# Kernel optimization log

Measured on AMD Instinct MI355X. Metric: run time of the kernel, lower is better.

## Reference

```python
import jax, jax.numpy as jnp
import numpy as np

N, IN_DIM, D, H, OUT = 4096, 512, 256, 256, 128


def setup_inputs() -> dict:
    key = jax.random.key(0)
    ks = jax.random.split(key, 12)
    s = 0.05
    x = jax.random.normal(ks[0], (N, IN_DIM), dtype=jnp.float32)
    # sparse-ish dense adjacency mask (avg degree ~80), int since only adj>0 is used
    adj = (jax.random.uniform(ks[1], (N, N)) < 0.02).astype(jnp.int32)
    return {
        "x": x,
        "adj": adj,
        "lin1_w": jax.random.normal(ks[2], (D, IN_DIM), dtype=jnp.float32) * s,
        "lin1_b": jax.random.normal(ks[3], (D,), dtype=jnp.float32) * s,
        "gat_W": jax.random.normal(ks[4], (D, D), dtype=jnp.float32) * s,
        "a_self": jax.random.normal(ks[5], (D,), dtype=jnp.float32) * s,
        "a_neigh": jax.random.normal(ks[6], (D,), dtype=jnp.float32) * s,
        "W_ih": jax.random.normal(ks[7], (4 * H, D), dtype=jnp.float32) * s,
        "W_hh": jax.random.normal(ks[8], (4 * H, H), dtype=jnp.float32) * s,
        "lin2_w": jax.random.normal(ks[9], (OUT, D), dtype=jnp.float32) * s,
        "lin2_b": jax.random.normal(ks[10], (OUT,), dtype=jnp.float32) * s,
    }


def reference(x, adj, lin1_w, lin1_b, gat_W, a_self, a_neigh, W_ih, W_hh, lin2_w, lin2_b):
    M = jnp.float32(0.2)        # scalar M passed by EWNELayer
    LRELU_SLOPE = 0.2           # alpha given to GraphAttentionLayer
    NEG_INF = jnp.float32(-9e15)

    # lin1
    x1 = x @ lin1_w.T + lin1_b                       # [N, D]

    # --- GraphAttentionLayer (DAEGC-style, dense adjacency mask) ---
    h = x1 @ gat_W                                   # [N, D]
    e = (h @ a_self)[:, None] + (h @ a_neigh)[None, :]  # [N, N]
    e = jax.nn.leaky_relu(e * M, LRELU_SLOPE)
    scores = jnp.where(adj > 0, e, NEG_INF)
    attn = jax.nn.softmax(scores, axis=1)            # [N, N]
    h_prime = attn @ h                               # [N, D]
    g = jnp.tanh(jax.nn.elu(h_prime))                # ELU (concat=True) then tanh

    # --- single-timestep LSTM, no bias, h0 = c0 = 0 ---
    h0 = jnp.zeros((N, H), dtype=g.dtype)
    c0 = jnp.zeros((N, H), dtype=g.dtype)
    gates = g @ W_ih.T + h0 @ W_hh.T                 # [N, 4H], torch order i,f,g,o
    i_g, f_g, g_g, o_g = jnp.split(gates, 4, axis=1)
    i_g = jax.nn.sigmoid(i_g)
    f_g = jax.nn.sigmoid(f_g)
    g_g = jnp.tanh(g_g)
    o_g = jax.nn.sigmoid(o_g)
    c1 = f_g * c0 + i_g * g_g
    h1 = o_g * jnp.tanh(c1)                          # [N, H]

    # lin2 -> normalize -> dot-product decode
    out = h1 @ lin2_w.T + lin2_b                     # [N, OUT]
    norm = jnp.maximum(jnp.linalg.norm(out, axis=1, keepdims=True), 1e-12)
    z = out / norm
    A_pred = jax.nn.sigmoid(z @ z.T)                 # [N, N]
    return A_pred, z, out
```

## Files before the change

### kernel.cpp

```cpp
#include <hip/hip_runtime.h>

#define NN_ 4096
#define IN_DIM_ 512
#define D_ 256
#define OUT_ 128
#define MAXC 320

typedef unsigned short u16;
typedef unsigned int u32;
typedef __attribute__((ext_vector_type(8))) short short8;
typedef __attribute__((ext_vector_type(4))) float f32x4;
typedef __attribute__((ext_vector_type(4))) int i32x4;

union U16x8 { uint4 u4; short8 s8; };

__device__ __forceinline__ u16 f2bf(float f){
  u32 u = __builtin_bit_cast(u32, f);
  u = (u + 0x7FFFu + ((u >> 16) & 1u)) >> 16;
  return (u16)u;
}
__device__ __forceinline__ float bf2f(u16 u){ return __builtin_bit_cast(float, ((u32)u) << 16); }
__device__ __forceinline__ float sigm(float v){ return __fdividef(1.f, 1.f + __expf(-v)); }

__device__ __forceinline__ void mfma_mainloop(const u16* __restrict__ A,
    const u16* __restrict__ B, int K, int ldA, int ldB, int row0, int col0,
    uint4* As, uint4* Bs, f32x4 acc[4][4], int tid) {
  const int wave = tid >> 6, lane = tid & 63;
  const int wm = wave >> 1, wn = wave & 1;
  const int r16 = lane & 15, kg = lane >> 4;
  for (int k0 = 0; k0 < K; k0 += 64) {
    #pragma unroll
    for (int i = 0; i < 4; i++) {
      int id = tid + (i << 8);
      int r = id >> 3, cc = id & 7;
      As[(r << 3) + (cc ^ (r & 7))] = *(const uint4*)(A + (size_t)(row0 + r) * ldA + k0 + cc * 8);
      Bs[(r << 3) + (cc ^ (r & 7))] = *(const uint4*)(B + (size_t)(col0 + r) * ldB + k0 + cc * 8);
    }
    __syncthreads();
    #pragma unroll
    for (int ks = 0; ks < 2; ks++) {
      int kb = (ks << 2) + kg;
      U16x8 a[4], b[4];
      #pragma unroll
      for (int m2 = 0; m2 < 4; m2++) {
        int r = (wm << 6) + (m2 << 4) + r16;
        a[m2].u4 = As[(r << 3) + (kb ^ (r & 7))];
      }
      #pragma unroll
      for (int n2 = 0; n2 < 4; n2++) {
        int r = (wn << 6) + (n2 << 4) + r16;
        b[n2].u4 = Bs[(r << 3) + (kb ^ (r & 7))];
      }
      #pragma unroll
      for (int m2 = 0; m2 < 4; m2++)
        #pragma unroll
        for (int n2 = 0; n2 < 4; n2++)
          acc[m2][n2] = __builtin_amdgcn_mfma_f32_16x16x32_bf16(
              a[m2].s8, b[n2].s8, acc[m2][n2], 0, 0, 0);
    }
    __syncthreads();
  }
}

__global__ __launch_bounds__(256) void prep_kernel(
    const float* __restrict__ lin1_w, const float* __restrict__ gat_W,
    const float* __restrict__ lin1_b,
    u16* __restrict__ WcT_bf, float* __restrict__ bcomb) {
  __shared__ __align__(16) float As[32][36];
  __shared__ __align__(16) float Bs[32][36];
  const int b = blockIdx.x, tid = threadIdx.x;
  if (b < 128) {
    const int m0 = (b & 15) << 5;
    const int n0 = (b >> 4) << 5;
    const int tx = tid & 15, ty = tid >> 4;
    float acc[2][2] = {};
    for (int k0 = 0; k0 < 256; k0 += 32) {
      int kk = tid >> 3, c4 = (tid & 7) << 2;
      *(float4*)&As[kk][c4] = *(const float4*)(lin1_w + (size_t)(k0 + kk) * 512 + m0 + c4);
      *(float4*)&Bs[kk][c4] = *(const float4*)(gat_W + (size_t)(k0 + kk) * 256 + n0 + c4);
      __syncthreads();
      #pragma unroll
      for (int k2 = 0; k2 < 32; k2++) {
        float a0 = As[k2][(ty << 1)], a1 = As[k2][(ty << 1) + 1];
        float b0 = Bs[k2][(tx << 1)], b1 = Bs[k2][(tx << 1) + 1];
        acc[0][0] = __builtin_fmaf(a0, b0, acc[0][0]);
        acc[0][1] = __builtin_fmaf(a0, b1, acc[0][1]);
        acc[1][0] = __builtin_fmaf(a1, b0, acc[1][0]);
        acc[1][1] = __builtin_fmaf(a1, b1, acc[1][1]);
      }
      __syncthreads();
    }
    #pragma unroll
    for (int r = 0; r < 2; r++)
      #pragma unroll
      for (int c = 0; c < 2; c++)
        WcT_bf[(size_t)(n0 + (tx << 1) + c) * 512 + m0 + (ty << 1) + r] = f2bf(acc[r][c]);
  } else {
    float a = 0.f;
    #pragma unroll 8
    for (int d = 0; d < 256; d++)
      a = __builtin_fmaf(lin1_b[d], gat_W[(size_t)d * 256 + tid], a);
    bcomb[tid] = a;
  }
}

__global__ __launch_bounds__(256) void hgemm_st_kernel(const float* __restrict__ x,
    const u16* __restrict__ WcT, const float* __restrict__ bias,
    const float* __restrict__ a_self, const float* __restrict__ a_nei,
    const float* __restrict__ W_ih, const float* __restrict__ lin2_w,
    const int* __restrict__ adj,
    u16* __restrict__ h_bf, float* __restrict__ s, float* __restrict__ t,
    u16* __restrict__ Wihp_bf, u16* __restrict__ l2w_bf,
    u16* __restrict__ nidxg, int* __restrict__ cnt) {
  __shared__ uint4 As[16 * 8];
  __shared__ uint4 Bs[256 * 8];
  __shared__ float sred[4][16];
  __shared__ float tred[4][16];
  __shared__ int wtot4[4];
  const int tid = threadIdx.x;
  int b = blockIdx.x;
  if (b >= 480) {
    const int row = b - 480;
    const int lane = tid & 63, wave = tid >> 6;
    const i32x4* arow = (const i32x4*)(adj + (size_t)row * NN_);
    i32x4 a4[4];
    #pragma unroll
    for (int i = 0; i < 4; i++) a4[i] = __builtin_nontemporal_load(&arow[(i << 8) + tid]);
    int vals[16];
    #pragma unroll
    for (int i = 0; i < 4; i++)
      #pragma unroll
      for (int q = 0; q < 4; q++) vals[(i << 2) + q] = a4[i][q];
    int c = 0;
    #pragma unroll
    for (int q = 0; q < 16; q++) c += (vals[q] > 0);
    int pref = c;
    #pragma unroll
    for (int off = 1; off < 64; off <<= 1) {
      int u = __shfl_up(pref, off);
      if (lane >= off) pref += u;
    }
    if (lane == 63) wtot4[wave] = pref;
    __syncthreads();
    int woff = 0;
    #pragma unroll
    for (int w = 0; w < 4; w++) woff += (w < wave) ? wtot4[w] : 0;
    int n = wtot4[0] + wtot4[1] + wtot4[2] + wtot4[3];
    int p = woff + pref - c;
    #pragma unroll
    for (int i = 0; i < 4; i++)
      #pragma unroll
      for (int q = 0; q < 4; q++) {
        if (vals[(i << 2) + q] > 0) {
          int j = (i << 10) + (tid << 2) + q;
          if (p < MAXC) nidxg[(size_t)row * MAXC + p] = (u16)j;
          p++;
        }
      }
    if (tid == 0) cnt[row] = n;
    return;
  }
  if (b >= 256) {
    b -= 256;
    if (b < 192) {
      int r = (b << 2) + (tid >> 6);
      int grp = r / 48, rem = r - grp * 48;
      int gidx = rem >> 4, hcl = rem & 15;
      int gate = (gidx == 0) ? 0 : ((gidx == 1) ? 2 : 3);
      int orig = gate * 256 + grp * 16 + hcl;
      int k = (tid & 63) << 2;
      float4 v = *(const float4*)(W_ih + (size_t)orig * 256 + k);
      ushort4 o = {f2bf(v.x), f2bf(v.y), f2bf(v.z), f2bf(v.w)};
      *(ushort4*)(Wihp_bf + (size_t)r * 256 + k) = o;
    } else {
      int off = (b - 192) * 1024 + tid * 4;
      float4 v = *(const float4*)(lin2_w + off);
      ushort4 o = {f2bf(v.x), f2bf(v.y), f2bf(v.z), f2bf(v.w)};
      *(ushort4*)(l2w_bf + off) = o;
    }
    return;
  }
  const int row0 = b << 4;
  const int wave = tid >> 6, lane = tid & 63;
  const int r16 = lane & 15, kg = lane >> 4;
  f32x4 acc[4];
  #pragma unroll
  for (int n2 = 0; n2 < 4; n2++) acc[n2] = (f32x4){0.f,0.f,0.f,0.f};
  for (int k0 = 0; k0 < IN_DIM_; k0 += 64) {
    if (tid < 128) {
      int r = tid >> 3, cc = tid & 7;
      const float* src = x + (size_t)(row0 + r) * IN_DIM_ + k0 + cc * 8;
      float4 lo = *(const float4*)src;
      float4 hi = *(const float4*)(src + 4);
      u16 e[8] = {f2bf(lo.x), f2bf(lo.y), f2bf(lo.z), f2bf(lo.w),
                  f2bf(hi.x), f2bf(hi.y), f2bf(hi.z), f2bf(hi.w)};
      As[(r << 3) + (cc ^ (r & 7))] = *(uint4*)e;
    }
    #pragma unroll
    for (int i = 0; i < 8; i++) {
      int id = tid + (i << 8);
      int r = id >> 3, cc = id & 7;
      Bs[(r << 3) + (cc ^ (r & 7))] = *(const uint4*)(WcT + (size_t)r * IN_DIM_ + k0 + cc * 8);
    }
    __syncthreads();
    #pragma unroll
    for (int ks = 0; ks < 2; ks++) {
      int kb = (ks << 2) + kg;
      U16x8 a, bb[4];
      a.u4 = As[(r16 << 3) + (kb ^ (r16 & 7))];
      #pragma unroll
      for (int n2 = 0; n2 < 4; n2++) {
        int r = (wave << 6) + (n2 << 4) + r16;
        bb[n2].u4 = Bs[(r << 3) + (kb ^ (r & 7))];
      }
      #pragma unroll
      for (int n2 = 0; n2 < 4; n2++)
        acc[n2] = __builtin_amdgcn_mfma_f32_16x16x32_bf16(a.s8, bb[n2].s8, acc[n2], 0, 0, 0);
    }
    __syncthreads();
  }
  float ps[4] = {0.f,0.f,0.f,0.f}, pt[4] = {0.f,0.f,0.f,0.f};
  #pragma unroll
  for (int n2 = 0; n2 < 4; n2++) {
    int col = (wave << 6) + (n2 << 4) + r16;
    float as = a_self[col], an = a_nei[col], bs = bias[col];
    #pragma unroll
    for (int q = 0; q < 4; q++) {
      float v = acc[n2][q] + bs;
      h_bf[(size_t)(row0 + (kg << 2) + q) * D_ + col] = f2bf(v);
      ps[q] = __builtin_fmaf(v, as, ps[q]);
      pt[q] = __builtin_fmaf(v, an, pt[q]);
    }
  }
  #pragma unroll
  for (int q = 0; q < 4; q++) {
    #pragma unroll
    for (int off = 8; off; off >>= 1) {
      ps[q] += __shfl_xor(ps[q], off);
      pt[q] += __shfl_xor(pt[q], off);
    }
  }
  if (r16 == 0) {
    #pragma unroll
    for (int q = 0; q < 4; q++) {
      sred[wave][(kg << 2) + q] = ps[q];
      tred[wave][(kg << 2) + q] = pt[q];
    }
  }
  __syncthreads();
  if (tid < 16)
    s[row0 + tid] = sred[0][tid] + sred[1][tid] + sred[2][tid] + sred[3][tid];
  else if (tid < 32)
    t[row0 + tid - 16] = tred[0][tid-16] + tred[1][tid-16] + tred[2][tid-16] + tred[3][tid-16];
}

__global__ __launch_bounds__(256) void attn4_kernel(const u16* __restrict__ nidxg,
    const int* __restrict__ cnt, const u16* __restrict__ h_bf,
    const float* __restrict__ s, const float* __restrict__ t,
    u16* __restrict__ g_bf) {
  __shared__ int nidx[MAXC];
  __shared__ float ne[MAXC];
  __shared__ float red[4][256];
  __shared__ float reds[4];
  const int tid = threadIdx.x;
  const int row = blockIdx.x;
  const int lane = tid & 63, wave = tid >> 6;
  int n = cnt[row];
  if (n > MAXC) n = MAXC;
  const float si = s[row];
  float ls = 0.f;
  for (int k = tid; k < n; k += 256) {
    int j = nidxg[(size_t)row * MAXC + k];
    float e = 0.2f * (si + t[j]);
    e = e > 0.f ? e : 0.2f * e;
    float wgt = __expf(e);
    nidx[k] = j; ne[k] = wgt; ls += wgt;
  }
  #pragma unroll
  for (int off = 32; off; off >>= 1) ls += __shfl_xor(ls, off);
  if (lane == 0) reds[wave] = ls;
  __syncthreads();
  float S = reds[0] + reds[1] + reds[2] + reds[3];
  const int hl = lane & 31, ksel = lane >> 5;
  float acc[8] = {0.f, 0.f, 0.f, 0.f, 0.f, 0.f, 0.f, 0.f};
  #pragma unroll 4
  for (int k = (wave << 1) + ksel; k < n; k += 8) {
    float wgt = ne[k];
    int j = nidx[k];
    U16x8 hv; hv.u4 = *(const uint4*)(h_bf + ((size_t)j << 8) + (hl << 3));
    #pragma unroll
    for (int q = 0; q < 8; q++)
      acc[q] = __builtin_fmaf(wgt, bf2f((u16)hv.s8[q]), acc[q]);
  }
  #pragma unroll
  for (int q = 0; q < 8; q++) acc[q] += __shfl_down(acc[q], 32);
  if (lane < 32) {
    #pragma unroll
    for (int q = 0; q < 8; q++) red[wave][(hl << 3) + q] = acc[q];
  }
  __syncthreads();
  float hp;
  if (n > 0) {
    hp = (red[0][tid] + red[1][tid] + red[2][tid] + red[3][tid]) / S;
  } else {
    float a2 = 0.f;
    for (int j = 0; j < NN_; j++) a2 += bf2f(h_bf[((size_t)j << 8) + tid]);
    hp = a2 / NN_;
  }
  float el = hp > 0.f ? hp : __expf(hp) - 1.f;
  g_bf[((size_t)row << 8) + tid] = f2bf(tanhf(el));
}

__global__ __launch_bounds__(256) void gates_lstm_kernel(const u16* __restrict__ A,
    const u16* __restrict__ B, u16* __restrict__ h1b) {
  __shared__ uint4 As[128 * 8];
  __shared__ uint4 Bs[96 * 8];
  const int tid = threadIdx.x;
  const int row0 = blockIdx.y << 7;
  const int col0 = blockIdx.x * 96;
  const int wave = tid >> 6, lane = tid & 63;
  const int wm = wave >> 1, wn = wave & 1;
  const int r16 = lane & 15, kg = lane >> 4;
  f32x4 acc[4][3];
  #pragma unroll
  for (int m2 = 0; m2 < 4; m2++)
    #pragma unroll
    for (int n2 = 0; n2 < 3; n2++) acc[m2][n2] = (f32x4){0.f,0.f,0.f,0.f};
  for (int k0 = 0; k0 < D_; k0 += 64) {
    #pragma unroll
    for (int i = 0; i < 4; i++) {
      int id = tid + (i << 8);
      int r = id >> 3, cc = id & 7;
      As[(r << 3) + (cc ^ (r & 7))] = *(const uint4*)(A + (size_t)(row0 + r) * D_ + k0 + cc * 8);
    }
    #pragma unroll
    for (int i = 0; i < 3; i++) {
      int id = tid + (i << 8);
      int r = id >> 3, cc = id & 7;
      Bs[(r << 3) + (cc ^ (r & 7))] = *(const uint4*)(B + (size_t)(col0 + r) * D_ + k0 + cc * 8);
    }
    __syncthreads();
    #pragma unroll
    for (int ks = 0; ks < 2; ks++) {
      int kb = (ks << 2) + kg;
      U16x8 a[4], bb[3];
      #pragma unroll
      for (int m2 = 0; m2 < 4; m2++) {
        int r = (wm << 6) + (m2 << 4) + r16;
        a[m2].u4 = As[(r << 3) + (kb ^ (r & 7))];
      }
      #pragma unroll
      for (int n2 = 0; n2 < 3; n2++) {
        int r = wn * 48 + (n2 << 4) + r16;
        bb[n2].u4 = Bs[(r << 3) + (kb ^ (r & 7))];
      }
      #pragma unroll
      for (int m2 = 0; m2 < 4; m2++)
        #pragma unroll
        for (int n2 = 0; n2 < 3; n2++)
          acc[m2][n2] = __builtin_amdgcn_mfma_f32_16x16x32_bf16(
              a[m2].s8, bb[n2].s8, acc[m2][n2], 0, 0, 0);
    }
    __syncthreads();
  }
  const int hc = ((blockIdx.x << 1) + wn) * 16 + r16;
  #pragma unroll
  for (int m2 = 0; m2 < 4; m2++)
    #pragma unroll
    for (int q = 0; q < 4; q++) {
      size_t grow = row0 + (wm << 6) + (m2 << 4) + (kg << 2) + q;
      float ig = acc[m2][0][q], gg = acc[m2][1][q], og = acc[m2][2][q];
      float c1 = sigm(ig) * tanhf(gg);
      h1b[grow * D_ + hc] = f2bf(sigm(og) * tanhf(c1));
    }
}

__global__ __launch_bounds__(256) void lin2f_kernel(const u16* __restrict__ A,
    const u16* __restrict__ B, const float* __restrict__ bias,
    float* __restrict__ out, float* __restrict__ z, u16* __restrict__ zb) {
  __shared__ uint4 As[16 * 8];
  __shared__ uint4 Bs[128 * 8];
  __shared__ float ssred[4][16];
  const int tid = threadIdx.x;
  const int wave = tid >> 6, lane = tid & 63;
  const int r16 = lane & 15, kg = lane >> 4;
  const int row0 = blockIdx.x << 4;
  f32x4 acc[2];
  acc[0] = (f32x4){0.f,0.f,0.f,0.f}; acc[1] = (f32x4){0.f,0.f,0.f,0.f};
  for (int k0 = 0; k0 < D_; k0 += 64) {
    if (tid < 128) {
      int r = tid >> 3, cc = tid & 7;
      As[(r << 3) + (cc ^ (r & 7))] = *(const uint4*)(A + (size_t)(row0 + r) * D_ + k0 + cc * 8);
    }
    #pragma unroll
    for (int i = 0; i < 4; i++) {
      int id = tid + (i << 8);
      int r = id >> 3, cc = id & 7;
      Bs[(r << 3) + (cc ^ (r & 7))] = *(const uint4*)(B + (size_t)r * D_ + k0 + cc * 8);
    }
    __syncthreads();
    #pragma unroll
    for (int ks = 0; ks < 2; ks++) {
      int kb = (ks << 2) + kg;
      U16x8 a, bb[2];
      a.u4 = As[(r16 << 3) + (kb ^ (r16 & 7))];
      #pragma unroll
      for (int n2 = 0; n2 < 2; n2++) {
        int r = (wave << 5) + (n2 << 4) + r16;
        bb[n2].u4 = Bs[(r << 3) + (kb ^ (r & 7))];
      }
      #pragma unroll
      for (int n2 = 0; n2 < 2; n2++)
        acc[n2] = __builtin_amdgcn_mfma_f32_16x16x32_bf16(a.s8, bb[n2].s8, acc[n2], 0, 0, 0);
    }
    __syncthreads();
  }
  float v[2][4], ss[4];
  #pragma unroll
  for (int q = 0; q < 4; q++) ss[q] = 0.f;
  #pragma unroll
  for (int n2 = 0; n2 < 2; n2++) {
    int col = (wave << 5) + (n2 << 4) + r16;
    float bs = bias[col];
    #pragma unroll
    for (int q = 0; q < 4; q++) {
      float vv = acc[n2][q] + bs;
      v[n2][q] = vv;
      ss[q] = __builtin_fmaf(vv, vv, ss[q]);
    }
  }
  #pragma unroll
  for (int q = 0; q < 4; q++)
    #pragma unroll
    for (int off = 8; off; off >>= 1) ss[q] += __shfl_xor(ss[q], off);
  if (r16 == 0) {
    #pragma unroll
    for (int q = 0; q < 4; q++) ssred[wave][(kg << 2) + q] = ss[q];
  }
  __syncthreads();
  #pragma unroll
  for (int q = 0; q < 4; q++) {
    int rrow = (kg << 2) + q;
    float tot = ssred[0][rrow] + ssred[1][rrow] + ssred[2][rrow] + ssred[3][rrow];
    float inv = __fdividef(1.f, fmaxf(sqrtf(tot), 1e-12f));
    size_t grow = row0 + rrow;
    #pragma unroll
    for (int n2 = 0; n2 < 2; n2++) {
      int col = (wave << 5) + (n2 << 4) + r16;
      float vv = v[n2][q], zz = vv * inv;
      out[grow * OUT_ + col] = vv;
      z[grow * OUT_ + col] = zz;
      zb[grow * OUT_ + col] = f2bf(zz);
    }
  }
}

__global__ __launch_bounds__(256) void decode_kernel(const u16* __restrict__ zb,
    float* __restrict__ C) {
  __shared__ uint4 As[128 * 8];
  __shared__ uint4 Bs[128 * 8];
  const int tid = threadIdx.x;
  const int row0 = blockIdx.y << 7, col0 = blockIdx.x << 7;
  f32x4 acc[4][4];
  #pragma unroll
  for (int m2 = 0; m2 < 4; m2++)
    #pragma unroll
    for (int n2 = 0; n2 < 4; n2++) acc[m2][n2] = (f32x4){0.f,0.f,0.f,0.f};
  mfma_mainloop(zb, zb, OUT_, OUT_, OUT_, row0, col0, As, Bs, acc, tid);
  const int wave = tid >> 6, lane = tid & 63;
  const int r16 = lane & 15, kg = lane >> 4;
  const int orow = row0 + ((wave >> 1) << 6), ocol = col0 + ((wave & 1) << 6);
  #pragma unroll
  for (int m2 = 0; m2 < 4; m2++)
    #pragma unroll
    for (int n2 = 0; n2 < 4; n2++)
      #pragma unroll
      for (int q = 0; q < 4; q++) {
        size_t gr = orow + (m2 << 4) + (kg << 2) + q;
        int gc = ocol + (n2 << 4) + r16;
        C[gr * NN_ + gc] = sigm(acc[m2][n2][q]);
      }
}

extern "C" void kernel_launch(void* const* d_in, const int* in_sizes, int n_in,
                              void* d_out, int out_size, void* d_ws, size_t ws_size,
                              hipStream_t stream) {
  const float* x      = (const float*)d_in[0];
  const int*   adj    = (const int*)  d_in[1];
  const float* lin1_w = (const float*)d_in[2];
  const float* lin1_b = (const float*)d_in[3];
  const float* gat_W  = (const float*)d_in[4];
  const float* a_self = (const float*)d_in[5];
  const float* a_nei  = (const float*)d_in[6];
  const float* W_ih   = (const float*)d_in[7];
  const float* lin2_w = (const float*)d_in[9];
  const float* lin2_b = (const float*)d_in[10];

  float* A_pred = (float*)d_out;
  float* z_out  = A_pred + (size_t)NN_ * NN_;
  float* out_o  = z_out + (size_t)NN_ * OUT_;

  char* w = (char*)d_ws;
  u16* h_bf    = (u16*)w;
  u16* g_bf    = (u16*)(w + (2u << 20));
  u16* h1_bf   = (u16*)(w + (4u << 20));
  u16* zb      = (u16*)(w + (6u << 20));
  u16* Wihp_bf = (u16*)(w + (7u << 20));
  u16* WcT_bf  = (u16*)(w + (7u << 20) + (384u << 10));
  u16* l2w_bf  = (u16*)(w + (7u << 20) + (640u << 10));
  float* bcomb = (float*)(w + (7u << 20) + (704u << 10));
  float* s     = (float*)(w + (7u << 20) + (768u << 10));
  float* t     = (float*)(w + (7u << 20) + (832u << 10));
  u16* nidxg   = (u16*)(w + (8u << 20));
  int* cnt     = (int*)(w + (11u << 20));

  prep_kernel<<<dim3(129), dim3(256), 0, stream>>>(
      lin1_w, gat_W, lin1_b, WcT_bf, bcomb);
  hgemm_st_kernel<<<dim3(4576), dim3(256), 0, stream>>>(
      x, WcT_bf, bcomb, a_self, a_nei, W_ih, lin2_w, adj,
      h_bf, s, t, Wihp_bf, l2w_bf, nidxg, cnt);
  attn4_kernel<<<dim3(4096), dim3(256), 0, stream>>>(nidxg, cnt, h_bf, s, t, g_bf);
  gates_lstm_kernel<<<dim3(8, 32), dim3(256), 0, stream>>>(g_bf, Wihp_bf, h1_bf);
  lin2f_kernel<<<dim3(256), dim3(256), 0, stream>>>(h1_bf, l2w_bf, lin2_b, out_o, z_out, zb);
  decode_kernel<<<dim3(32, 32), dim3(256), 0, stream>>>(zb, A_pred);
}
```

Before: 80.09 us.

## Fuse LSTM gates GEMM with lin2/normalize kernel keeping h1 in LDS

Merges the gates+LSTM GEMM and the lin2+L2-normalize GEMM into one 512-thread kernel that processes 64 rows per block. The h1 activations stay in shared memory instead of a global round trip, and one kernel launch is removed. It also reorders the hgemm_st grid so the adjacency-compaction blocks come first. The catch is only 64 blocks on a large GPU, so parallelism is low and there is more LDS per block.

```diff
diff --git a/kernel.cpp b/kernel.cpp
--- a/kernel.cpp
+++ b/kernel.cpp
@@ -119,8 +119,8 @@
   __shared__ int wtot4[4];
   const int tid = threadIdx.x;
   int b = blockIdx.x;
-  if (b >= 480) {
-    const int row = b - 480;
+  if (b < 4096) {
+    const int row = b;
     const int lane = tid & 63, wave = tid >> 6;
     const i32x4* arow = (const i32x4*)(adj + (size_t)row * NN_);
     i32x4 a4[4];
@@ -160,6 +160,7 @@
     if (tid == 0) cnt[row] = n;
     return;
   }
+  b -= 4096;
   if (b >= 256) {
     b -= 256;
     if (b < 192) {
@@ -311,148 +312,170 @@
   g_bf[((size_t)row << 8) + tid] = f2bf(tanhf(el));
 }
 
-__global__ __launch_bounds__(256) void gates_lstm_kernel(const u16* __restrict__ A,
-    const u16* __restrict__ B, u16* __restrict__ h1b) {
-  __shared__ uint4 As[128 * 8];
-  __shared__ uint4 Bs[96 * 8];
-  const int tid = threadIdx.x;
-  const int row0 = blockIdx.y << 7;
-  const int col0 = blockIdx.x * 96;
-  const int wave = tid >> 6, lane = tid & 63;
-  const int wm = wave >> 1, wn = wave & 1;
-  const int r16 = lane & 15, kg = lane >> 4;
-  f32x4 acc[4][3];
-  #pragma unroll
-  for (int m2 = 0; m2 < 4; m2++)
-    #pragma unroll
-    for (int n2 = 0; n2 < 3; n2++) acc[m2][n2] = (f32x4){0.f,0.f,0.f,0.f};
-  for (int k0 = 0; k0 < D_; k0 += 64) {
-    #pragma unroll
-    for (int i = 0; i < 4; i++) {
-      int id = tid + (i << 8);
-      int r = id >> 3, cc = id & 7;
-      As[(r << 3) + (cc ^ (r & 7))] = *(const uint4*)(A + (size_t)(row0 + r) * D_ + k0 + cc * 8);
-    }
-    #pragma unroll
-    for (int i = 0; i < 3; i++) {
-      int id = tid + (i << 8);
-      int r = id >> 3, cc = id & 7;
-      Bs[(r << 3) + (cc ^ (r & 7))] = *(const uint4*)(B + (size_t)(col0 + r) * D_ + k0 + cc * 8);
-    }
-    __syncthreads();
-    #pragma unroll
-    for (int ks = 0; ks < 2; ks++) {
-      int kb = (ks << 2) + kg;
-      U16x8 a[4], bb[3];
-      #pragma unroll
-      for (int m2 = 0; m2 < 4; m2++) {
-        int r = (wm << 6) + (m2 << 4) + r16;
-        a[m2].u4 = As[(r << 3) + (kb ^ (r & 7))];
-      }
-      #pragma unroll
-      for (int n2 = 0; n2 < 3; n2++) {
-        int r = wn * 48 + (n2 << 4) + r16;
-        bb[n2].u4 = Bs[(r << 3) + (kb ^ (r & 7))];
-      }
-      #pragma unroll
-      for (int m2 = 0; m2 < 4; m2++)
-        #pragma unroll
-        for (int n2 = 0; n2 < 3; n2++)
-          acc[m2][n2] = __builtin_amdgcn_mfma_f32_16x16x32_bf16(
-              a[m2].s8, bb[n2].s8, acc[m2][n2], 0, 0, 0);
-    }
-    __syncthreads();
-  }
-  const int hc = ((blockIdx.x << 1) + wn) * 16 + r16;
-  #pragma unroll
-  for (int m2 = 0; m2 < 4; m2++)
-    #pragma unroll
-    for (int q = 0; q < 4; q++) {
-      size_t grow = row0 + (wm << 6) + (m2 << 4) + (kg << 2) + q;
-      float ig = acc[m2][0][q], gg = acc[m2][1][q], og = acc[m2][2][q];
-      float c1 = sigm(ig) * tanhf(gg);
-      h1b[grow * D_ + hc] = f2bf(sigm(og) * tanhf(c1));
-    }
-}
-
-__global__ __launch_bounds__(256) void lin2f_kernel(const u16* __restrict__ A,
-    const u16* __restrict__ B, const float* __restrict__ bias,
-    float* __restrict__ out, float* __restrict__ z, u16* __restrict__ zb) {
-  __shared__ uint4 As[16 * 8];
-  __shared__ uint4 Bs[128 * 8];
-  __shared__ float ssred[4][16];
+__global__ __launch_bounds__(512) void glf_kernel(const u16* __restrict__ g_bf,
+    const u16* __restrict__ Wihp, const u16* __restrict__ l2w,
+    const float* __restrict__ bias, float* __restrict__ out,
+    float* __restrict__ z, u16* __restrict__ zb) {
+  __shared__ uint4 As[64 * 32];
+  __shared__ uint4 Bs[384 * 8];
+  __shared__ u16 h1s[64 * 256];
+  __shared__ float ssred[8][32];
   const int tid = threadIdx.x;
   const int wave = tid >> 6, lane = tid & 63;
+  const int wm = wave >> 2, wn = wave & 3;
   const int r16 = lane & 15, kg = lane >> 4;
-  const int row0 = blockIdx.x << 4;
-  f32x4 acc[2];
-  acc[0] = (f32x4){0.f,0.f,0.f,0.f}; acc[1] = (f32x4){0.f,0.f,0.f,0.f};
+  const int r0 = blockIdx.x << 6;
+  #pragma unroll
+  for (int i = 0; i < 4; i++) {
+    int e = tid + (i << 9);
+    int r = e >> 5, kb = e & 31;
+    As[(r << 5) + (kb ^ (r & 7))] = *(const uint4*)(g_bf + (size_t)(r0 + r) * D_ + kb * 8);
+  }
+  for (int p = 0; p < 2; p++) {
+    f32x4 acc[2][6];
+    #pragma unroll
+    for (int m2 = 0; m2 < 2; m2++)
+      #pragma unroll
+      for (int n2 = 0; n2 < 6; n2++) acc[m2][n2] = (f32x4){0.f,0.f,0.f,0.f};
+    for (int k0 = 0; k0 < D_; k0 += 64) {
+      #pragma unroll
+      for (int i = 0; i < 6; i++) {
+        int e = tid + (i << 9);
+        int r = e >> 3, c8 = e & 7;
+        Bs[(r << 3) + (c8 ^ (r & 7))] =
+            *(const uint4*)(Wihp + (size_t)(p * 384 + r) * D_ + k0 + c8 * 8);
+      }
+      __syncthreads();
+      #pragma unroll
+      for (int ks = 0; ks < 2; ks++) {
+        int kbi = (k0 >> 3) + (ks << 2) + kg;
+        int kb8 = (ks << 2) + kg;
+        U16x8 a[2], bb[6];
+        #pragma unroll
+        for (int m2 = 0; m2 < 2; m2++) {
+          int r = (wm << 5) + (m2 << 4) + r16;
+          a[m2].u4 = As[(r << 5) + (kbi ^ (r & 7))];
+        }
+        #pragma unroll
+        for (int n2 = 0; n2 < 6; n2++) {
+          int rl = wn * 96 + (n2 << 4) + r16;
+          bb[n2].u4 = Bs[(rl << 3) + (kb8 ^ (rl & 7))];
+        }
+        #pragma unroll
+        for (int m2 = 0; m2 < 2; m2++)
+          #pragma unroll
+          for (int n2 = 0; n2 < 6; n2++)
+            acc[m2][n2] = __builtin_amdgcn_mfma_f32_16x16x32_bf16(
+                a[m2].s8, bb[n2].s8, acc[m2][n2], 0, 0, 0);
+      }
+      __syncthreads();
+    }
+    #pragma unroll
+    for (int m2 = 0; m2 < 2; m2++)
+      #pragma unroll
+      for (int g2 = 0; g2 < 2; g2++) {
+        int hc = (((p << 3) + (wn << 1) + g2) << 4) + r16;
+        int u = hc >> 3, sub = hc & 7;
+        #pragma unroll
+        for (int q = 0; q < 4; q++) {
+          int r = (wm << 5) + (m2 << 4) + (kg << 2) + q;
+          float i_ = acc[m2][g2 * 3 + 0][q];
+          float g_ = acc[m2][g2 * 3 + 1][q];
+          float o_ = acc[m2][g2 * 3 + 2][q];
+          float c1 = sigm(i_) * tanhf(g_);
+          h1s[((r << 5) + (u ^ (r & 7))) * 8 + sub] = f2bf(sigm(o_) * tanhf(c1));
+        }
+      }
+  }
+  __syncthreads();
+  const uint4* h1v = (const uint4*)h1s;
+  f32x4 acc2[2][2];
+  #pragma unroll
+  for (int m2 = 0; m2 < 2; m2++)
+    #pragma unroll
+    for (int n2 = 0; n2 < 2; n2++) acc2[m2][n2] = (f32x4){0.f,0.f,0.f,0.f};
   for (int k0 = 0; k0 < D_; k0 += 64) {
-    if (tid < 128) {
-      int r = tid >> 3, cc = tid & 7;
-      As[(r << 3) + (cc ^ (r & 7))] = *(const uint4*)(A + (size_t)(row0 + r) * D_ + k0 + cc * 8);
-    }
-    #pragma unroll
-    for (int i = 0; i < 4; i++) {
-      int id = tid + (i << 8);
-      int r = id >> 3, cc = id & 7;
-      Bs[(r << 3) + (cc ^ (r & 7))] = *(const uint4*)(B + (size_t)r * D_ + k0 + cc * 8);
+    #pragma unroll
+    for (int i = 0; i < 2; i++) {
+      int e = tid + (i << 9);
+      int r = e >> 3, c8 = e & 7;
+      Bs[(r << 3) + (c8 ^ (r & 7))] = *(const uint4*)(l2w + (size_t)r * D_ + k0 + c8 * 8);
     }
     __syncthreads();
     #pragma unroll
     for (int ks = 0; ks < 2; ks++) {
-      int kb = (ks << 2) + kg;
-      U16x8 a, bb[2];
-      a.u4 = As[(r16 << 3) + (kb ^ (r16 & 7))];
+      int kbi = (k0 >> 3) + (ks << 2) + kg;
+      int kb8 = (ks << 2) + kg;
+      U16x8 a[2], bb[2];
+      #pragma unroll
+      for (int m2 = 0; m2 < 2; m2++) {
+        int r = (wm << 5) + (m2 << 4) + r16;
+        a[m2].u4 = h1v[(r << 5) + (kbi ^ (r & 7))];
+      }
       #pragma unroll
       for (int n2 = 0; n2 < 2; n2++) {
-        int r = (wave << 5) + (n2 << 4) + r16;
-        bb[n2].u4 = Bs[(r << 3) + (kb ^ (r & 7))];
-      }
-      #pragma unroll
-      for (int n2 = 0; n2 < 2; n2++)
-        acc[n2] = __builtin_amdgcn_mfma_f32_16x16x32_bf16(a.s8, bb[n2].s8, acc[n2], 0, 0, 0);
-    }
-    __syncthreads();
-  }
-  float v[2][4], ss[4];
-  #pragma unroll
-  for (int q = 0; q < 4; q++) ss[q] = 0.f;
-  #pragma unroll
-  for (int n2 = 0; n2 < 2; n2++) {
-    int col = (wave << 5) + (n2 << 4) + r16;
-    float bs = bias[col];
+        int rl = (wn << 5) + (n2 << 4) + r16;
+        bb[n2].u4 = Bs[(rl << 3) + (kb8 ^ (rl & 7))];
+      }
+      #pragma unroll
+      for (int m2 = 0; m2 < 2; m2++)
+        #pragma unroll
+        for (int n2 = 0; n2 < 2; n2++)
+          acc2[m2][n2] = __builtin_amdgcn_mfma_f32_16x16x32_bf16(
+              a[m2].s8, bb[n2].s8, acc2[m2][n2], 0, 0, 0);
+    }
+    __syncthreads();
+  }
+  float v[2][2][4], ss[2][4];
+  #pragma unroll
+  for (int m2 = 0; m2 < 2; m2++)
+    #pragma unroll
+    for (int q = 0; q < 4; q++) ss[m2][q] = 0.f;
+  #pragma unroll
+  for (int m2 = 0; m2 < 2; m2++)
+    #pragma unroll
+    for (int n2 = 0; n2 < 2; n2++) {
+      int col = (wn << 5) + (n2 << 4) + r16;
+      float bs = bias[col];
+      #pragma unroll
+      for (int q = 0; q < 4; q++) {
+        float vv = acc2[m2][n2][q] + bs;
+        v[m2][n2][q] = vv;
+        ss[m2][q] = __builtin_fmaf(vv, vv, ss[m2][q]);
+      }
+    }
+  #pragma unroll
+  for (int m2 = 0; m2 < 2; m2++)
+    #pragma unroll
+    for (int q = 0; q < 4; q++)
+      #pragma unroll
+      for (int off = 8; off; off >>= 1) ss[m2][q] += __shfl_xor(ss[m2][q], off);
+  if (r16 == 0) {
+    #pragma unroll
+    for (int m2 = 0; m2 < 2; m2++)
+      #pragma unroll
+      for (int q = 0; q < 4; q++)
+        ssred[wave][(m2 << 4) + (kg << 2) + q] = ss[m2][q];
+  }
+  __syncthreads();
+  #pragma unroll
+  for (int m2 = 0; m2 < 2; m2++)
     #pragma unroll
     for (int q = 0; q < 4; q++) {
-      float vv = acc[n2][q] + bs;
-      v[n2][q] = vv;
-      ss[q] = __builtin_fmaf(vv, vv, ss[q]);
-    }
-  }
-  #pragma unroll
-  for (int q = 0; q < 4; q++)
-    #pragma unroll
-    for (int off = 8; off; off >>= 1) ss[q] += __shfl_xor(ss[q], off);
-  if (r16 == 0) {
-    #pragma unroll
-    for (int q = 0; q < 4; q++) ssred[wave][(kg << 2) + q] = ss[q];
-  }
-  __syncthreads();
-  #pragma unroll
-  for (int q = 0; q < 4; q++) {
-    int rrow = (kg << 2) + q;
-    float tot = ssred[0][rrow] + ssred[1][rrow] + ssred[2][rrow] + ssred[3][rrow];
-    float inv = __fdividef(1.f, fmaxf(sqrtf(tot), 1e-12f));
-    size_t grow = row0 + rrow;
-    #pragma unroll
-    for (int n2 = 0; n2 < 2; n2++) {
-      int col = (wave << 5) + (n2 << 4) + r16;
-      float vv = v[n2][q], zz = vv * inv;
-      out[grow * OUT_ + col] = vv;
-      z[grow * OUT_ + col] = zz;
-      zb[grow * OUT_ + col] = f2bf(zz);
-    }
-  }
+      int rl = (m2 << 4) + (kg << 2) + q;
+      float tot = ssred[(wm << 2)][rl] + ssred[(wm << 2) + 1][rl] +
+                  ssred[(wm << 2) + 2][rl] + ssred[(wm << 2) + 3][rl];
+      float inv = __fdividef(1.f, fmaxf(sqrtf(tot), 1e-12f));
+      size_t grow = r0 + (wm << 5) + rl;
+      #pragma unroll
+      for (int n2 = 0; n2 < 2; n2++) {
+        int col = (wn << 5) + (n2 << 4) + r16;
+        float vv = v[m2][n2][q], zz = vv * inv;
+        out[grow * OUT_ + col] = vv;
+        z[grow * OUT_ + col] = zz;
+        zb[grow * OUT_ + col] = f2bf(zz);
+      }
+    }
 }
 
 __global__ __launch_bounds__(256) void decode_kernel(const u16* __restrict__ zb,
@@ -503,16 +526,15 @@
   char* w = (char*)d_ws;
   u16* h_bf    = (u16*)w;
   u16* g_bf    = (u16*)(w + (2u << 20));
-  u16* h1_bf   = (u16*)(w + (4u << 20));
-  u16* zb      = (u16*)(w + (6u << 20));
-  u16* Wihp_bf = (u16*)(w + (7u << 20));
-  u16* WcT_bf  = (u16*)(w + (7u << 20) + (384u << 10));
-  u16* l2w_bf  = (u16*)(w + (7u << 20) + (640u << 10));
-  float* bcomb = (float*)(w + (7u << 20) + (704u << 10));
-  float* s     = (float*)(w + (7u << 20) + (768u << 10));
-  float* t     = (float*)(w + (7u << 20) + (832u << 10));
-  u16* nidxg   = (u16*)(w + (8u << 20));
-  int* cnt     = (int*)(w + (11u << 20));
+  u16* zb      = (u16*)(w + (4u << 20));
+  u16* Wihp_bf = (u16*)(w + (5u << 20));
+  u16* WcT_bf  = (u16*)(w + (5u << 20) + (384u << 10));
+  u16* l2w_bf  = (u16*)(w + (5u << 20) + (640u << 10));
+  float* bcomb = (float*)(w + (5u << 20) + (704u << 10));
+  float* s     = (float*)(w + (5u << 20) + (768u << 10));
+  float* t     = (float*)(w + (5u << 20) + (832u << 10));
+  u16* nidxg   = (u16*)(w + (6u << 20));
+  int* cnt     = (int*)(w + (9u << 20));
 
   prep_kernel<<<dim3(129), dim3(256), 0, stream>>>(
       lin1_w, gat_W, lin1_b, WcT_bf, bcomb);
@@ -520,7 +542,7 @@
       x, WcT_bf, bcomb, a_self, a_nei, W_ih, lin2_w, adj,
       h_bf, s, t, Wihp_bf, l2w_bf, nidxg, cnt);
   attn4_kernel<<<dim3(4096), dim3(256), 0, stream>>>(nidxg, cnt, h_bf, s, t, g_bf);
-  gates_lstm_kernel<<<dim3(8, 32), dim3(256), 0, stream>>>(g_bf, Wihp_bf, h1_bf);
-  lin2f_kernel<<<dim3(256), dim3(256), 0, stream>>>(h1_bf, l2w_bf, lin2_b, out_o, z_out, zb);
+  glf_kernel<<<dim3(64), dim3(512), 0, stream>>>(
+      g_bf, Wihp_bf, l2w_bf, lin2_b, out_o, z_out, zb);
   decode_kernel<<<dim3(32, 32), dim3(256), 0, stream>>>(zb, A_pred);
 }
```

Result: slower. 92.51 us (+15.5%).
